# Kernel optimization log

Measured on AMD Instinct MI355X. Metric: run time of the kernel, lower is better.

The kernel has to match this reference:

```python
import jax, jax.numpy as jnp
import numpy as np

B, K, T = 64, 256, 64      # batch, num_tokens (feature dim of e / Dense units), word tokens
DF, N = 768, 1024          # image feature channels, spatial regions


def setup_inputs() -> dict:
    key = jax.random.key(0)
    k1, k2, k3 = jax.random.split(key, 3)
    e = jax.random.normal(k1, (B, K, T), dtype=jnp.float32)
    f = jax.random.normal(k2, (B, DF, N), dtype=jnp.float32)
    # Dense(units=K) kernel/bias (Glorot-ish scale)
    W = jax.random.normal(k3, (DF, K), dtype=jnp.float32) / np.sqrt(DF)
    b = jnp.zeros((K,), dtype=jnp.float32)
    gamma = jnp.float32(5.0)  # DAMSM smoothing factor gamma1
    return {"e": e, "f": f, "gamma": gamma, "W": W, "b": b}


def reference(e, f, gamma, W, b):
    # v = transpose(Dense(transpose(f))): project image features Df -> K. [B,K,N]
    v = jnp.einsum('bdn,dk->bkn', f, W) + b[None, :, None]
    # attention scores between word tokens and regions: [B,T,N]
    s = jnp.einsum('bkt,bkn->btn', e, v)
    # gamma-scaled softmax over regions (axis=2)
    alpha = jax.nn.softmax(gamma * s, axis=2)
    # region-context vectors per token: [B,K,T]
    c = jnp.einsum('bkn,btn->bkt', v, alpha)
    # per-token feature norms (reduce over feature axis 1): [B,T]
    lc = jnp.sqrt(jnp.sum(c * c, axis=1))
    le = jnp.sqrt(jnp.sum(e * e, axis=1))
    # token-token cosine similarity: contract feature axis, normalize by outer(lc, le)
    cos = jnp.einsum('bki,bkj->bij', c, e) / (lc[:, :, None] * le[:, None, :])
    return cos
```

## Files before the change

kernel.cpp:

```cpp
#include <hip/hip_runtime.h>

#define B_  64
#define K_  256
#define T_  64
#define DF_ 768
#define N_  1024

typedef __attribute__((ext_vector_type(8))) short bf16x8;
typedef __attribute__((ext_vector_type(4))) float f32x4;

__device__ __forceinline__ unsigned short bf_rne(float x) {
    unsigned u = __float_as_uint(x);
    unsigned r = u + 0x7fffu + ((u >> 16) & 1u);
    return (unsigned short)(r >> 16);
}

__global__ __launch_bounds__(256) void prep_we(const float* __restrict__ W,
                                               const float* __restrict__ e,
                                               unsigned short* __restrict__ W_hi,
                                               unsigned short* __restrict__ W_lo,
                                               unsigned short* __restrict__ WT_hi,
                                               unsigned short* __restrict__ eT_hi,
                                               unsigned short* __restrict__ eT_lo) {
    int blk = blockIdx.x;
    if (blk < DF_) {
        int d = blk, k = threadIdx.x;
        float w = W[d * K_ + k];
        unsigned u = __float_as_uint(w);
        unsigned short hs = (unsigned short)(u >> 16);
        float hi = __uint_as_float(u & 0xffff0000u);
        W_hi[d * K_ + k]   = hs;
        W_lo[d * K_ + k]   = bf_rne(w - hi);
        WT_hi[k * DF_ + d] = hs;
    } else {
        int q = blk - DF_;
        int b = q >> 2, kq = q & 3;
        int t = threadIdx.x & 63, ko = threadIdx.x >> 6;
        const float* eb = e + (size_t)b * K_ * T_;
        unsigned short* eh = eT_hi + (size_t)b * T_ * K_;
        unsigned short* el = eT_lo + (size_t)b * T_ * K_;
#pragma unroll
        for (int i = 0; i < 16; i++) {
            int k = kq * 64 + ko * 16 + i;
            float x = eb[k * T_ + t];
            unsigned u = __float_as_uint(x);
            unsigned short hs = (unsigned short)(u >> 16);
            float hi = __uint_as_float(u & 0xffff0000u);
            eh[t * K_ + k] = hs;
            el[t * K_ + k] = bf_rne(x - hi);
        }
    }
}

__global__ __launch_bounds__(256, 2) void gemm_g(const unsigned short* __restrict__ eT_hi,
                                                 const unsigned short* __restrict__ eT_lo,
                                                 const unsigned short* __restrict__ W_hi,
                                                 const unsigned short* __restrict__ W_lo,
                                                 unsigned short* __restrict__ gT_hi,
                                                 unsigned short* __restrict__ gT_lo) {
    __shared__ unsigned short LeH[2][64 * 40], LeL[2][64 * 40];
    __shared__ unsigned short LwH[2][64 * 40], LwL[2][64 * 40];
    const int dblk = blockIdx.x * 64;
    const int b = blockIdx.y;
    const int tid = threadIdx.x;
    const int lane = tid & 63, w = tid >> 6, q = lane >> 4, l16 = lane & 15;

    const unsigned short* eh = eT_hi + (size_t)b * T_ * K_;
    const unsigned short* el = eT_lo + (size_t)b * T_ * K_;

    f32x4 acc[4];
#pragma unroll
    for (int i = 0; i < 4; i++) acc[i] = (f32x4)(0.f);

    const int tr = tid >> 2, c8 = (tid & 3) * 8;
    const unsigned short* ehp = eh + (size_t)tr * K_ + c8;
    const unsigned short* elp = el + (size_t)tr * K_ + c8;
    const unsigned short* whp = W_hi + (size_t)(dblk + tr) * K_ + c8;
    const unsigned short* wlp = W_lo + (size_t)(dblk + tr) * K_ + c8;

    uint4 peH, peL, pwH, pwL;
    auto gload = [&](int k0) {
        peH = *(const uint4*)&ehp[k0];
        peL = *(const uint4*)&elp[k0];
        pwH = *(const uint4*)&whp[k0];
        pwL = *(const uint4*)&wlp[k0];
    };
    auto gstore = [&](int buf) {
        *(uint4*)&LeH[buf][tr * 40 + c8] = peH;
        *(uint4*)&LeL[buf][tr * 40 + c8] = peL;
        *(uint4*)&LwH[buf][tr * 40 + c8] = pwH;
        *(uint4*)&LwL[buf][tr * 40 + c8] = pwL;
    };
    auto gcomp = [&](int buf) {
        bf16x8 aH[4], aL[4], bH, bL;
#pragma unroll
        for (int mt = 0; mt < 4; mt++) {
            aH[mt] = *(const bf16x8*)&LeH[buf][(mt * 16 + l16) * 40 + q * 8];
            aL[mt] = *(const bf16x8*)&LeL[buf][(mt * 16 + l16) * 40 + q * 8];
        }
        int dl = w * 16 + l16;
        bH = *(const bf16x8*)&LwH[buf][dl * 40 + q * 8];
        bL = *(const bf16x8*)&LwL[buf][dl * 40 + q * 8];
#pragma unroll
        for (int mt = 0; mt < 4; mt++) {
            acc[mt] = __builtin_amdgcn_mfma_f32_16x16x32_bf16(aH[mt], bH, acc[mt], 0, 0, 0);
            acc[mt] = __builtin_amdgcn_mfma_f32_16x16x32_bf16(aH[mt], bL, acc[mt], 0, 0, 0);
            acc[mt] = __builtin_amdgcn_mfma_f32_16x16x32_bf16(aL[mt], bH, acc[mt], 0, 0, 0);
        }
    };

    gload(0);
    gstore(0);
    __syncthreads();
    int cur = 0;
    for (int k0 = 0; k0 < K_ - 32; k0 += 32) {
        gload(k0 + 32);
        gcomp(cur);
        gstore(cur ^ 1);
        __syncthreads();
        cur ^= 1;
    }
    gcomp(cur);

    unsigned short* gh = gT_hi + (size_t)b * T_ * DF_;
    unsigned short* gl = gT_lo + (size_t)b * T_ * DF_;
#pragma unroll
    for (int mt = 0; mt < 4; mt++)
#pragma unroll
        for (int r = 0; r < 4; r++) {
            float x = acc[mt][r];
            int t = mt * 16 + q * 4 + r;
            int d = dblk + w * 16 + l16;
            unsigned u = __float_as_uint(x);
            unsigned short hs = (unsigned short)(u >> 16);
            float hi = __uint_as_float(u & 0xffff0000u);
            gh[t * DF_ + d] = hs;
            gl[t * DF_ + d] = bf_rne(x - hi);
        }
}

__global__ __launch_bounds__(256, 2) void gemm_s(const unsigned short* __restrict__ gT_hi,
                                                 const unsigned short* __restrict__ gT_lo,
                                                 const float* __restrict__ f,
                                                 float* __restrict__ s) {
    __shared__ unsigned short LgH[2][64 * 40], LgL[2][64 * 40];
    __shared__ unsigned LfH[2][128 * 20], LfL[2][128 * 20];

    const int flat = blockIdx.x;
    const int b    = (flat & 7) * 8 + ((flat >> 3) & 7);
    const int nblk = (flat >> 6) * 128;
    const int tid = threadIdx.x;
    const int lane = tid & 63, w = tid >> 6, q = lane >> 4, l16 = lane & 15;

    const unsigned short* gh = gT_hi + (size_t)b * T_ * DF_;
    const unsigned short* gl = gT_lo + (size_t)b * T_ * DF_;

    f32x4 acc[4][2];
#pragma unroll
    for (int i = 0; i < 4; i++)
#pragma unroll
        for (int j = 0; j < 2; j++) acc[i][j] = (f32x4)(0.f);

    const int dp  = tid >> 4;
    const int nb  = (tid & 15) * 8;
    const int rot = tid & 7;
    const int tr = tid >> 2, c8 = (tid & 3) * 8;

    const float* fbase = f + ((size_t)b * DF_ + dp * 2) * N_ + nblk + nb;
    const unsigned short* ghp = gh + (size_t)tr * DF_ + c8;
    const unsigned short* glp = gl + (size_t)tr * DF_ + c8;

    float4 px0, px1, py0, py1;
    uint4 pgH, pgL;

    auto sload = [&](int d0) {
        const float* fp = fbase + (size_t)d0 * N_;
        px0 = *(const float4*)&fp[0];
        px1 = *(const float4*)&fp[4];
        py0 = *(const float4*)&fp[N_ + 0];
        py1 = *(const float4*)&fp[N_ + 4];
        pgH = *(const uint4*)&ghp[d0];
        pgL = *(const uint4*)&glp[d0];
    };
    auto sstore = [&](int buf) {
        *(uint4*)&LgH[buf][tr * 40 + c8] = pgH;
        *(uint4*)&LgL[buf][tr * 40 + c8] = pgL;
        const float xs[8] = {px0.x, px0.y, px0.z, px0.w, px1.x, px1.y, px1.z, px1.w};
        const float ys[8] = {py0.x, py0.y, py0.z, py0.w, py1.x, py1.y, py1.z, py1.w};
#pragma unroll
        for (int jj = 0; jj < 8; jj++) {
            int j = (jj + rot) & 7;
            unsigned bx = __float_as_uint(xs[j]);
            unsigned by = __float_as_uint(ys[j]);
            unsigned hp = (bx >> 16) | (by & 0xffff0000u);
            float lx = xs[j] - __uint_as_float(bx & 0xffff0000u);
            float ly = ys[j] - __uint_as_float(by & 0xffff0000u);
            unsigned lp = (__float_as_uint(lx) >> 16) | (__float_as_uint(ly) & 0xffff0000u);
            LfH[buf][(nb + j) * 20 + dp] = hp;
            LfL[buf][(nb + j) * 20 + dp] = lp;
        }
    };
    auto scomp = [&](int buf) {
        bf16x8 aH[4], aL[4], bH[2], bL[2];
#pragma unroll
        for (int mt = 0; mt < 4; mt++) {
            aH[mt] = *(const bf16x8*)&LgH[buf][(mt * 16 + l16) * 40 + q * 8];
            aL[mt] = *(const bf16x8*)&LgL[buf][(mt * 16 + l16) * 40 + q * 8];
        }
#pragma unroll
        for (int nt = 0; nt < 2; nt++) {
            int nl = w * 32 + nt * 16 + l16;
            bH[nt] = *(const bf16x8*)&((const unsigned short*)LfH[buf])[nl * 40 + q * 8];
            bL[nt] = *(const bf16x8*)&((const unsigned short*)LfL[buf])[nl * 40 + q * 8];
        }
#pragma unroll
        for (int mt = 0; mt < 4; mt++)
#pragma unroll
            for (int nt = 0; nt < 2; nt++) {
                acc[mt][nt] = __builtin_amdgcn_mfma_f32_16x16x32_bf16(aH[mt], bH[nt], acc[mt][nt], 0, 0, 0);
                acc[mt][nt] = __builtin_amdgcn_mfma_f32_16x16x32_bf16(aH[mt], bL[nt], acc[mt][nt], 0, 0, 0);
                acc[mt][nt] = __builtin_amdgcn_mfma_f32_16x16x32_bf16(aL[mt], bH[nt], acc[mt][nt], 0, 0, 0);
            }
    };

    sload(0);
    sstore(0);
    __syncthreads();
    int cur = 0;
    for (int d0 = 0; d0 < DF_ - 32; d0 += 32) {
        sload(d0 + 32);
        scomp(cur);
        sstore(cur ^ 1);
        __syncthreads();
        cur ^= 1;
    }
    scomp(cur);

    float* sb = s + (size_t)b * T_ * N_;
#pragma unroll
    for (int mt = 0; mt < 4; mt++)
#pragma unroll
        for (int nt = 0; nt < 2; nt++)
#pragma unroll
            for (int r = 0; r < 4; r++) {
                int t = mt * 16 + q * 4 + r;
                int n = nblk + w * 32 + nt * 16 + l16;
                sb[(size_t)t * N_ + n] = acc[mt][nt][r];
            }
}

__global__ __launch_bounds__(256) void softmax_k(const float* __restrict__ s,
                                                 unsigned short* __restrict__ alpha,
                                                 const float* __restrict__ gptr) {
    const float g = gptr[0];
    const int row_id = blockIdx.x * 4 + (threadIdx.x >> 6);
    const int lane = threadIdx.x & 63;
    const float* row = s + (size_t)row_id * N_;
    unsigned short* arow = alpha + (size_t)row_id * N_;

    float4 x[4];
#pragma unroll
    for (int i = 0; i < 4; i++) {
        x[i] = *(const float4*)(row + i * 256 + lane * 4);
        x[i].x *= g; x[i].y *= g; x[i].z *= g; x[i].w *= g;
    }
    float m = x[0].x;
#pragma unroll
    for (int i = 0; i < 4; i++)
        m = fmaxf(m, fmaxf(fmaxf(x[i].x, x[i].y), fmaxf(x[i].z, x[i].w)));
#pragma unroll
    for (int off = 32; off > 0; off >>= 1) m = fmaxf(m, __shfl_xor(m, off, 64));

    float ev[16];
    float sum = 0.f;
#pragma unroll
    for (int i = 0; i < 4; i++) {
        ev[i * 4 + 0] = __expf(x[i].x - m);
        ev[i * 4 + 1] = __expf(x[i].y - m);
        ev[i * 4 + 2] = __expf(x[i].z - m);
        ev[i * 4 + 3] = __expf(x[i].w - m);
        sum += ev[i * 4 + 0] + ev[i * 4 + 1] + ev[i * 4 + 2] + ev[i * 4 + 3];
    }
#pragma unroll
    for (int off = 32; off > 0; off >>= 1) sum += __shfl_xor(sum, off, 64);
    float inv = 1.f / sum;
#pragma unroll
    for (int i = 0; i < 4; i++) {
        unsigned p0 = (unsigned)bf_rne(ev[i * 4 + 0] * inv) | ((unsigned)bf_rne(ev[i * 4 + 1] * inv) << 16);
        unsigned p1 = (unsigned)bf_rne(ev[i * 4 + 2] * inv) | ((unsigned)bf_rne(ev[i * 4 + 3] * inv) << 16);
        uint2 o; o.x = p0; o.y = p1;
        *(uint2*)&arow[i * 256 + lane * 4] = o;
    }
}

__global__ __launch_bounds__(256, 2) void gemm_h(const float* __restrict__ f,
                                                 const unsigned short* __restrict__ alpha,
                                                 unsigned short* __restrict__ hT) {
    __shared__ unsigned short Lf[2][64 * 72];
    __shared__ unsigned short La[2][64 * 72];
    const int dblk = blockIdx.x * 64;
    const int b = blockIdx.y;
    const int tid = threadIdx.x;
    const int lane = tid & 63, w = tid >> 6, q = lane >> 4, l16 = lane & 15;

    const float* fb = f + (size_t)b * DF_ * N_;
    const unsigned short* ab = alpha + (size_t)b * T_ * N_;

    f32x4 acc[4];
#pragma unroll
    for (int i = 0; i < 4; i++) acc[i] = (f32x4)(0.f);

    const int fr_ = tid >> 2, fc = tid & 3;
    const float* frbase = fb + (size_t)(dblk + fr_) * N_ + fc * 16;
    const unsigned short* abase = ab + (size_t)fr_ * N_ + fc * 16;

    float4 pf0, pf1, pf2, pf3;
    uint4 pa0, pa1;

    auto hload = [&](int n0) {
        const float* fp = frbase + n0;
        pf0 = *(const float4*)&fp[0];
        pf1 = *(const float4*)&fp[4];
        pf2 = *(const float4*)&fp[8];
        pf3 = *(const float4*)&fp[12];
        pa0 = *(const uint4*)&abase[n0];
        pa1 = *(const uint4*)&abase[n0 + 8];
    };
    auto hstore = [&](int buf) {
        const float4 fx[4] = {pf0, pf1, pf2, pf3};
#pragma unroll
        for (int i = 0; i < 4; i++) {
            float4 x = fx[i];
            unsigned p0 = (unsigned)bf_rne(x.x) | ((unsigned)bf_rne(x.y) << 16);
            unsigned p1 = (unsigned)bf_rne(x.z) | ((unsigned)bf_rne(x.w) << 16);
            uint2 o; o.x = p0; o.y = p1;
            *(uint2*)&Lf[buf][fr_ * 72 + fc * 16 + i * 4] = o;
        }
        *(uint4*)&La[buf][fr_ * 72 + fc * 16]     = pa0;
        *(uint4*)&La[buf][fr_ * 72 + fc * 16 + 8] = pa1;
    };
    auto hcomp = [&](int buf) {
        bf16x8 af[2], bb[4][2];
#pragma unroll
        for (int kk = 0; kk < 2; kk++)
            af[kk] = *(const bf16x8*)&Lf[buf][(w * 16 + l16) * 72 + kk * 32 + q * 8];
#pragma unroll
        for (int nt = 0; nt < 4; nt++)
#pragma unroll
            for (int kk = 0; kk < 2; kk++)
                bb[nt][kk] = *(const bf16x8*)&La[buf][(nt * 16 + l16) * 72 + kk * 32 + q * 8];
#pragma unroll
        for (int nt = 0; nt < 4; nt++)
#pragma unroll
            for (int kk = 0; kk < 2; kk++)
                acc[nt] = __builtin_amdgcn_mfma_f32_16x16x32_bf16(af[kk], bb[nt][kk], acc[nt], 0, 0, 0);
    };

    hload(0);
    hstore(0);
    __syncthreads();
    int cur = 0;
    for (int n0 = 0; n0 < N_ - 64; n0 += 64) {
        hload(n0 + 64);
        hcomp(cur);
        hstore(cur ^ 1);
        __syncthreads();
        cur ^= 1;
    }
    hcomp(cur);

    unsigned short* hb = hT + (size_t)b * T_ * DF_;
#pragma unroll
    for (int nt = 0; nt < 4; nt++)
#pragma unroll
        for (int r = 0; r < 4; r++) {
            int d = dblk + w * 16 + q * 4 + r;
            int t = nt * 16 + l16;
            hb[(size_t)t * DF_ + d] = bf_rne(acc[nt][r]);
        }
}

__global__ __launch_bounds__(256, 2) void gemm_c(const unsigned short* __restrict__ WT_hi,
                                                 const unsigned short* __restrict__ hT,
                                                 const float* __restrict__ bias,
                                                 float* __restrict__ c) {
    __shared__ unsigned short LW[2][64 * 72];
    __shared__ unsigned short Lh[2][64 * 72];
    const int kblk = blockIdx.x * 64;
    const int b = blockIdx.y;
    const int tid = threadIdx.x;
    const int lane = tid & 63, w = tid >> 6, q = lane >> 4, l16 = lane & 15;

    const unsigned short* hb = hT + (size_t)b * T_ * DF_;

    f32x4 acc[4];
#pragma unroll
    for (int i = 0; i < 4; i++) acc[i] = (f32x4)(0.f);

    const int r_ = tid >> 2, cc = (tid & 3) * 16;
    const unsigned short* wbase = WT_hi + (size_t)(kblk + r_) * DF_ + cc;
    const unsigned short* hbase = hb + (size_t)r_ * DF_ + cc;

    uint4 pw0, pw1, ph0, ph1;
    auto cload = [&](int d0) {
        pw0 = *(const uint4*)&wbase[d0];
        pw1 = *(const uint4*)&wbase[d0 + 8];
        ph0 = *(const uint4*)&hbase[d0];
        ph1 = *(const uint4*)&hbase[d0 + 8];
    };
    auto cstore = [&](int buf) {
        *(uint4*)&LW[buf][r_ * 72 + cc]     = pw0;
        *(uint4*)&LW[buf][r_ * 72 + cc + 8] = pw1;
        *(uint4*)&Lh[buf][r_ * 72 + cc]     = ph0;
        *(uint4*)&Lh[buf][r_ * 72 + cc + 8] = ph1;
    };
    auto ccomp = [&](int buf) {
        bf16x8 aw[2], bh[4][2];
#pragma unroll
        for (int kk = 0; kk < 2; kk++)
            aw[kk] = *(const bf16x8*)&LW[buf][(w * 16 + l16) * 72 + kk * 32 + q * 8];
#pragma unroll
        for (int nt = 0; nt < 4; nt++)
#pragma unroll
            for (int kk = 0; kk < 2; kk++)
                bh[nt][kk] = *(const bf16x8*)&Lh[buf][(nt * 16 + l16) * 72 + kk * 32 + q * 8];
#pragma unroll
        for (int nt = 0; nt < 4; nt++)
#pragma unroll
            for (int kk = 0; kk < 2; kk++)
                acc[nt] = __builtin_amdgcn_mfma_f32_16x16x32_bf16(aw[kk], bh[nt][kk], acc[nt], 0, 0, 0);
    };

    cload(0);
    cstore(0);
    __syncthreads();
    int cur = 0;
    for (int d0 = 0; d0 < DF_ - 64; d0 += 64) {
        cload(d0 + 64);
        ccomp(cur);
        cstore(cur ^ 1);
        __syncthreads();
        cur ^= 1;
    }
    ccomp(cur);

    float* cb = c + (size_t)b * K_ * T_;
#pragma unroll
    for (int nt = 0; nt < 4; nt++)
#pragma unroll
        for (int r = 0; r < 4; r++) {
            int k = kblk + w * 16 + q * 4 + r;
            int t = nt * 16 + l16;
            cb[(size_t)k * T_ + t] = acc[nt][r] + bias[k];
        }
}

__global__ __launch_bounds__(256) void cos_k(const float* __restrict__ c,
                                             const float* __restrict__ e,
                                             float* __restrict__ out) {
    const int iq = threadIdx.x >> 6;
    const int i = blockIdx.x * 4 + iq;
    const int b = blockIdx.y;
    const int j = threadIdx.x & 63;
    const float* cb = c + (size_t)b * K_ * T_;
    const float* eb = e + (size_t)b * K_ * T_;

    float dot = 0.f, se = 0.f, sc = 0.f;
#pragma unroll 8
    for (int k = 0; k < K_; k++) {
        float cv = cb[(size_t)k * T_ + i];
        float ev = eb[(size_t)k * T_ + j];
        dot += cv * ev;
        se  += ev * ev;
        sc  += cv * cv;
    }
    out[((size_t)b * T_ + i) * T_ + j] = dot * rsqrtf(sc * se);
}

extern "C" void kernel_launch(void* const* d_in, const int* in_sizes, int n_in,
                              void* d_out, int out_size, void* d_ws, size_t ws_size,
                              hipStream_t stream) {
    const float* e     = (const float*)d_in[0];
    const float* f     = (const float*)d_in[1];
    const float* gamma = (const float*)d_in[2];
    const float* W     = (const float*)d_in[3];
    const float* bias  = (const float*)d_in[4];
    float* out = (float*)d_out;

    char* p = (char*)d_ws;
    unsigned short* W_hi  = (unsigned short*)p; p += (size_t)DF_ * K_ * 2;
    unsigned short* W_lo  = (unsigned short*)p; p += (size_t)DF_ * K_ * 2;
    unsigned short* WT_hi = (unsigned short*)p; p += (size_t)DF_ * K_ * 2;
    unsigned short* eT_hi = (unsigned short*)p; p += (size_t)B_ * T_ * K_ * 2;
    unsigned short* eT_lo = (unsigned short*)p; p += (size_t)B_ * T_ * K_ * 2;
    unsigned short* gT_hi = (unsigned short*)p; p += (size_t)B_ * T_ * DF_ * 2;
    unsigned short* gT_lo = (unsigned short*)p; p += (size_t)B_ * T_ * DF_ * 2;
    float*          s     = (float*)p;          p += (size_t)B_ * T_ * N_ * 4;
    unsigned short* alpha = (unsigned short*)p; p += (size_t)B_ * T_ * N_ * 2;
    unsigned short* hT    = (unsigned short*)p; p += (size_t)B_ * T_ * DF_ * 2;
    float*          c     = (float*)p;          p += (size_t)B_ * K_ * T_ * 4;

    prep_we <<<dim3(DF_ + 256),      256, 0, stream>>>(W, e, W_hi, W_lo, WT_hi, eT_hi, eT_lo);
    gemm_g  <<<dim3(DF_ / 64, B_),   256, 0, stream>>>(eT_hi, eT_lo, W_hi, W_lo, gT_hi, gT_lo);
    gemm_s  <<<dim3(512),            256, 0, stream>>>(gT_hi, gT_lo, f, s);
    softmax_k<<<dim3(B_ * T_ / 4),   256, 0, stream>>>(s, alpha, gamma);
    gemm_h  <<<dim3(DF_ / 64, B_),   256, 0, stream>>>(f, alpha, hT);
    gemm_c  <<<dim3(K_ / 64, B_),    256, 0, stream>>>(WT_hi, hT, bias, c);
    cos_k   <<<dim3(T_ / 4, B_),     256, 0, stream>>>(c, e, out);
}
```

Measured before the change: 377.1 us.

## Fuse softmax into score GEMM epilogue and consumer via split max/sum partials

Removes the standalone softmax kernel. The score GEMM now scales by gamma, writes scores, and emits per-tile row max and exp-sum partials through a shared LDS pool. The next GEMM combines the eight partials per row and recomputes exp on the fly while staging alpha into LDS. This drops one launch and the alpha buffer round trip, at the cost of reading fp32 scores instead of bf16 alpha (twice the bytes) and extra exp work in the consumer's staging path.

```diff
diff --git a/kernel.cpp b/kernel.cpp
--- a/kernel.cpp
+++ b/kernel.cpp
@@ -142,15 +142,23 @@
 __global__ __launch_bounds__(256, 2) void gemm_s(const unsigned short* __restrict__ gT_hi,
                                                  const unsigned short* __restrict__ gT_lo,
                                                  const float* __restrict__ f,
-                                                 float* __restrict__ s) {
-    __shared__ unsigned short LgH[2][64 * 40], LgL[2][64 * 40];
-    __shared__ unsigned LfH[2][128 * 20], LfL[2][128 * 20];
+                                                 float* __restrict__ s,
+                                                 float2* __restrict__ mz,
+                                                 const float* __restrict__ gptr) {
+    __shared__ __align__(16) char lds_pool[61440];
+    unsigned short* LgH = (unsigned short*)(lds_pool);
+    unsigned short* LgL = (unsigned short*)(lds_pool + 10240);
+    unsigned*       LfH = (unsigned*)(lds_pool + 20480);
+    unsigned*       LfL = (unsigned*)(lds_pool + 40960);
 
     const int flat = blockIdx.x;
     const int b    = (flat & 7) * 8 + ((flat >> 3) & 7);
-    const int nblk = (flat >> 6) * 128;
+    const int blkid = flat >> 6;
+    const int nblk = blkid * 128;
     const int tid = threadIdx.x;
     const int lane = tid & 63, w = tid >> 6, q = lane >> 4, l16 = lane & 15;
+
+    const float gscale = gptr[0];
 
     const unsigned short* gh = gT_hi + (size_t)b * T_ * DF_;
     const unsigned short* gl = gT_lo + (size_t)b * T_ * DF_;
@@ -183,8 +191,8 @@
         pgL = *(const uint4*)&glp[d0];
     };
     auto sstore = [&](int buf) {
-        *(uint4*)&LgH[buf][tr * 40 + c8] = pgH;
-        *(uint4*)&LgL[buf][tr * 40 + c8] = pgL;
+        *(uint4*)&LgH[buf * 2560 + tr * 40 + c8] = pgH;
+        *(uint4*)&LgL[buf * 2560 + tr * 40 + c8] = pgL;
         const float xs[8] = {px0.x, px0.y, px0.z, px0.w, px1.x, px1.y, px1.z, px1.w};
         const float ys[8] = {py0.x, py0.y, py0.z, py0.w, py1.x, py1.y, py1.z, py1.w};
 #pragma unroll
@@ -196,22 +204,22 @@
             float lx = xs[j] - __uint_as_float(bx & 0xffff0000u);
             float ly = ys[j] - __uint_as_float(by & 0xffff0000u);
             unsigned lp = (__float_as_uint(lx) >> 16) | (__float_as_uint(ly) & 0xffff0000u);
-            LfH[buf][(nb + j) * 20 + dp] = hp;
-            LfL[buf][(nb + j) * 20 + dp] = lp;
+            LfH[buf * 2560 + (nb + j) * 20 + dp] = hp;
+            LfL[buf * 2560 + (nb + j) * 20 + dp] = lp;
         }
     };
     auto scomp = [&](int buf) {
         bf16x8 aH[4], aL[4], bH[2], bL[2];
 #pragma unroll
         for (int mt = 0; mt < 4; mt++) {
-            aH[mt] = *(const bf16x8*)&LgH[buf][(mt * 16 + l16) * 40 + q * 8];
-            aL[mt] = *(const bf16x8*)&LgL[buf][(mt * 16 + l16) * 40 + q * 8];
+            aH[mt] = *(const bf16x8*)&LgH[buf * 2560 + (mt * 16 + l16) * 40 + q * 8];
+            aL[mt] = *(const bf16x8*)&LgL[buf * 2560 + (mt * 16 + l16) * 40 + q * 8];
         }
 #pragma unroll
         for (int nt = 0; nt < 2; nt++) {
             int nl = w * 32 + nt * 16 + l16;
-            bH[nt] = *(const bf16x8*)&((const unsigned short*)LfH[buf])[nl * 40 + q * 8];
-            bL[nt] = *(const bf16x8*)&((const unsigned short*)LfL[buf])[nl * 40 + q * 8];
+            bH[nt] = *(const bf16x8*)&((const unsigned short*)(LfH + buf * 2560))[nl * 40 + q * 8];
+            bL[nt] = *(const bf16x8*)&((const unsigned short*)(LfL + buf * 2560))[nl * 40 + q * 8];
         }
 #pragma unroll
         for (int mt = 0; mt < 4; mt++)
@@ -237,6 +245,8 @@
     scomp(cur);
 
     float* sb = s + (size_t)b * T_ * N_;
+    float* Ls = (float*)lds_pool;
+    __syncthreads();
 #pragma unroll
     for (int mt = 0; mt < 4; mt++)
 #pragma unroll
@@ -244,78 +254,75 @@
 #pragma unroll
             for (int r = 0; r < 4; r++) {
                 int t = mt * 16 + q * 4 + r;
-                int n = nblk + w * 32 + nt * 16 + l16;
-                sb[(size_t)t * N_ + n] = acc[mt][nt][r];
+                int nl = w * 32 + nt * 16 + l16;
+                float x = gscale * acc[mt][nt][r];
+                sb[(size_t)t * N_ + nblk + nl] = x;
+                Ls[t * 132 + nl] = x;
             }
-}
-
-__global__ __launch_bounds__(256) void softmax_k(const float* __restrict__ s,
-                                                 unsigned short* __restrict__ alpha,
-                                                 const float* __restrict__ gptr) {
-    const float g = gptr[0];
-    const int row_id = blockIdx.x * 4 + (threadIdx.x >> 6);
-    const int lane = threadIdx.x & 63;
-    const float* row = s + (size_t)row_id * N_;
-    unsigned short* arow = alpha + (size_t)row_id * N_;
-
-    float4 x[4];
-#pragma unroll
-    for (int i = 0; i < 4; i++) {
-        x[i] = *(const float4*)(row + i * 256 + lane * 4);
-        x[i].x *= g; x[i].y *= g; x[i].z *= g; x[i].w *= g;
-    }
-    float m = x[0].x;
-#pragma unroll
-    for (int i = 0; i < 4; i++)
-        m = fmaxf(m, fmaxf(fmaxf(x[i].x, x[i].y), fmaxf(x[i].z, x[i].w)));
-#pragma unroll
-    for (int off = 32; off > 0; off >>= 1) m = fmaxf(m, __shfl_xor(m, off, 64));
-
-    float ev[16];
-    float sum = 0.f;
-#pragma unroll
-    for (int i = 0; i < 4; i++) {
-        ev[i * 4 + 0] = __expf(x[i].x - m);
-        ev[i * 4 + 1] = __expf(x[i].y - m);
-        ev[i * 4 + 2] = __expf(x[i].z - m);
-        ev[i * 4 + 3] = __expf(x[i].w - m);
-        sum += ev[i * 4 + 0] + ev[i * 4 + 1] + ev[i * 4 + 2] + ev[i * 4 + 3];
-    }
-#pragma unroll
-    for (int off = 32; off > 0; off >>= 1) sum += __shfl_xor(sum, off, 64);
-    float inv = 1.f / sum;
-#pragma unroll
-    for (int i = 0; i < 4; i++) {
-        unsigned p0 = (unsigned)bf_rne(ev[i * 4 + 0] * inv) | ((unsigned)bf_rne(ev[i * 4 + 1] * inv) << 16);
-        unsigned p1 = (unsigned)bf_rne(ev[i * 4 + 2] * inv) | ((unsigned)bf_rne(ev[i * 4 + 3] * inv) << 16);
-        uint2 o; o.x = p0; o.y = p1;
-        *(uint2*)&arow[i * 256 + lane * 4] = o;
+    __syncthreads();
+    {
+        int t = tid >> 2, n0s = (tid & 3) * 32;
+        float vb[32];
+        float m = -3.4e38f;
+#pragma unroll
+        for (int jj = 0; jj < 8; jj++) {
+            float4 v4 = *(const float4*)&Ls[t * 132 + n0s + jj * 4];
+            vb[jj * 4 + 0] = v4.x; vb[jj * 4 + 1] = v4.y;
+            vb[jj * 4 + 2] = v4.z; vb[jj * 4 + 3] = v4.w;
+            m = fmaxf(m, fmaxf(fmaxf(v4.x, v4.y), fmaxf(v4.z, v4.w)));
+        }
+        float z = 0.f;
+#pragma unroll
+        for (int j2 = 0; j2 < 32; j2++) z += __expf(vb[j2] - m);
+        float om = m;
+        m = fmaxf(m, __shfl_xor(m, 1, 64));
+        m = fmaxf(m, __shfl_xor(m, 2, 64));
+        z *= __expf(om - m);
+        z += __shfl_xor(z, 1, 64);
+        z += __shfl_xor(z, 2, 64);
+        if ((tid & 3) == 0)
+            mz[((size_t)b * T_ + t) * 8 + blkid] = make_float2(m, z);
     }
 }
 
 __global__ __launch_bounds__(256, 2) void gemm_h(const float* __restrict__ f,
-                                                 const unsigned short* __restrict__ alpha,
+                                                 const float* __restrict__ s,
+                                                 const float2* __restrict__ mz,
                                                  unsigned short* __restrict__ hT) {
     __shared__ unsigned short Lf[2][64 * 72];
     __shared__ unsigned short La[2][64 * 72];
+    __shared__ float sM[64], sI[64];
     const int dblk = blockIdx.x * 64;
     const int b = blockIdx.y;
     const int tid = threadIdx.x;
     const int lane = tid & 63, w = tid >> 6, q = lane >> 4, l16 = lane & 15;
 
     const float* fb = f + (size_t)b * DF_ * N_;
-    const unsigned short* ab = alpha + (size_t)b * T_ * N_;
 
     f32x4 acc[4];
 #pragma unroll
     for (int i = 0; i < 4; i++) acc[i] = (f32x4)(0.f);
+
+    if (tid < 64) {
+        const float2* mzp = mz + ((size_t)b * T_ + tid) * 8;
+        float2 p0 = mzp[0], p1 = mzp[1], p2 = mzp[2], p3 = mzp[3];
+        float2 p4 = mzp[4], p5 = mzp[5], p6 = mzp[6], p7 = mzp[7];
+        float M = fmaxf(fmaxf(fmaxf(p0.x, p1.x), fmaxf(p2.x, p3.x)),
+                        fmaxf(fmaxf(p4.x, p5.x), fmaxf(p6.x, p7.x)));
+        float Z = p0.y * __expf(p0.x - M) + p1.y * __expf(p1.x - M) +
+                  p2.y * __expf(p2.x - M) + p3.y * __expf(p3.x - M) +
+                  p4.y * __expf(p4.x - M) + p5.y * __expf(p5.x - M) +
+                  p6.y * __expf(p6.x - M) + p7.y * __expf(p7.x - M);
+        sM[tid] = M;
+        sI[tid] = 1.f / Z;
+    }
 
     const int fr_ = tid >> 2, fc = tid & 3;
     const float* frbase = fb + (size_t)(dblk + fr_) * N_ + fc * 16;
-    const unsigned short* abase = ab + (size_t)fr_ * N_ + fc * 16;
+    const float* srbase = s + ((size_t)b * T_ + fr_) * N_ + fc * 16;
 
     float4 pf0, pf1, pf2, pf3;
-    uint4 pa0, pa1;
+    float4 ps0, ps1, ps2, ps3;
 
     auto hload = [&](int n0) {
         const float* fp = frbase + n0;
@@ -323,11 +330,20 @@
         pf1 = *(const float4*)&fp[4];
         pf2 = *(const float4*)&fp[8];
         pf3 = *(const float4*)&fp[12];
-        pa0 = *(const uint4*)&abase[n0];
-        pa1 = *(const uint4*)&abase[n0 + 8];
-    };
+        const float* sp = srbase + n0;
+        ps0 = *(const float4*)&sp[0];
+        ps1 = *(const float4*)&sp[4];
+        ps2 = *(const float4*)&sp[8];
+        ps3 = *(const float4*)&sp[12];
+    };
+
+    hload(0);
+    __syncthreads();
+    const float rowM = sM[fr_], rowI = sI[fr_];
+
     auto hstore = [&](int buf) {
         const float4 fx[4] = {pf0, pf1, pf2, pf3};
+        const float4 sx[4] = {ps0, ps1, ps2, ps3};
 #pragma unroll
         for (int i = 0; i < 4; i++) {
             float4 x = fx[i];
@@ -335,9 +351,17 @@
             unsigned p1 = (unsigned)bf_rne(x.z) | ((unsigned)bf_rne(x.w) << 16);
             uint2 o; o.x = p0; o.y = p1;
             *(uint2*)&Lf[buf][fr_ * 72 + fc * 16 + i * 4] = o;
-        }
-        *(uint4*)&La[buf][fr_ * 72 + fc * 16]     = pa0;
-        *(uint4*)&La[buf][fr_ * 72 + fc * 16 + 8] = pa1;
+
+            float4 sv = sx[i];
+            float a0 = __expf(sv.x - rowM) * rowI;
+            float a1 = __expf(sv.y - rowM) * rowI;
+            float a2 = __expf(sv.z - rowM) * rowI;
+            float a3 = __expf(sv.w - rowM) * rowI;
+            unsigned q0 = (unsigned)bf_rne(a0) | ((unsigned)bf_rne(a1) << 16);
+            unsigned q1 = (unsigned)bf_rne(a2) | ((unsigned)bf_rne(a3) << 16);
+            uint2 oa; oa.x = q0; oa.y = q1;
+            *(uint2*)&La[buf][fr_ * 72 + fc * 16 + i * 4] = oa;
+        }
     };
     auto hcomp = [&](int buf) {
         bf16x8 af[2], bb[4][2];
@@ -356,7 +380,6 @@
                 acc[nt] = __builtin_amdgcn_mfma_f32_16x16x32_bf16(af[kk], bb[nt][kk], acc[nt], 0, 0, 0);
     };
 
-    hload(0);
     hstore(0);
     __syncthreads();
     int cur = 0;
@@ -496,15 +519,14 @@
     unsigned short* gT_hi = (unsigned short*)p; p += (size_t)B_ * T_ * DF_ * 2;
     unsigned short* gT_lo = (unsigned short*)p; p += (size_t)B_ * T_ * DF_ * 2;
     float*          s     = (float*)p;          p += (size_t)B_ * T_ * N_ * 4;
-    unsigned short* alpha = (unsigned short*)p; p += (size_t)B_ * T_ * N_ * 2;
+    float2*         mz    = (float2*)p;         p += (size_t)B_ * T_ * 8 * sizeof(float2);
     unsigned short* hT    = (unsigned short*)p; p += (size_t)B_ * T_ * DF_ * 2;
     float*          c     = (float*)p;          p += (size_t)B_ * K_ * T_ * 4;
 
     prep_we <<<dim3(DF_ + 256),      256, 0, stream>>>(W, e, W_hi, W_lo, WT_hi, eT_hi, eT_lo);
     gemm_g  <<<dim3(DF_ / 64, B_),   256, 0, stream>>>(eT_hi, eT_lo, W_hi, W_lo, gT_hi, gT_lo);
-    gemm_s  <<<dim3(512),            256, 0, stream>>>(gT_hi, gT_lo, f, s);
-    softmax_k<<<dim3(B_ * T_ / 4),   256, 0, stream>>>(s, alpha, gamma);
-    gemm_h  <<<dim3(DF_ / 64, B_),   256, 0, stream>>>(f, alpha, hT);
+    gemm_s  <<<dim3(512),            256, 0, stream>>>(gT_hi, gT_lo, f, s, mz, gamma);
+    gemm_h  <<<dim3(DF_ / 64, B_),   256, 0, stream>>>(f, s, mz, hT);
     gemm_c  <<<dim3(K_ / 64, B_),    256, 0, stream>>>(WT_hi, hT, bias, c);
     cos_k   <<<dim3(T_ / 4, B_),     256, 0, stream>>>(c, e, out);
 }
```

New measurement: 374.9 us. About the same (-0.6%).
